# Performance work log

Measured on AMD Instinct MI355X. Metric: run time of the kernel, lower is better.

Reference implementation:

```python
import jax, jax.numpy as jnp
import numpy as np
from jax import lax

M = 5           # top-m similarities per (same/diff) group
MU = 2048       # number of confident target samples kept
K = 10          # top-k src neighbors for pseudo-label voting
NUM_CLASSES = 31
N, D = 4096, 256


def setup_inputs() -> dict:
    key = jax.random.key(0)
    k1, k2, k3 = jax.random.split(key, 3)
    return {
        "src_features": jax.random.normal(k1, (N, D), dtype=jnp.float32),
        "src_labels": jax.random.randint(k2, (N,), 0, NUM_CLASSES),
        "tgt_features": jax.random.normal(k3, (N, D), dtype=jnp.float32),
    }


def _forward(src_features, tgt_features, src_labels):
    # sim = 1 / (cdist(src, tgt) + 1), shape [Ns, Nt]
    sq_s = jnp.sum(src_features * src_features, axis=1, keepdims=True)   # [Ns,1]
    sq_t = jnp.sum(tgt_features * tgt_features, axis=1, keepdims=True)   # [Nt,1]
    d2 = jnp.maximum(sq_s + sq_t.T - 2.0 * (src_features @ tgt_features.T), 0.0)
    sim = 1.0 / (jnp.sqrt(d2) + 1.0)                                     # [Ns,Nt]

    # --- target pseudo-labels: majority vote among top-K most similar src samples per tgt column
    _, top_idx = lax.top_k(sim.T, K)                                     # [Nt,K] over src dim
    top_lab = src_labels[top_idx]                                        # [Nt,K]
    counts = jnp.sum(jax.nn.one_hot(top_lab, NUM_CLASSES, dtype=jnp.float32), axis=1)  # [Nt,C]
    # argmax returns smallest class index on ties, matching torch.mode
    assigned = jnp.argmax(counts, axis=1)                                # [Nt]

    # --- similarity-ratio confidence score per target
    same = src_labels[:, None] == assigned[None, :]                      # [Ns,Nt]
    # sims are strictly positive, so masking with 0 preserves the per-group top-M
    nln_sum = jnp.sum(lax.top_k(jnp.where(same, sim, 0.0).T, M)[0], axis=-1)   # [Nt]
    nun_sum = jnp.sum(lax.top_k(jnp.where(same, 0.0, sim).T, M)[0], axis=-1)   # [Nt]
    score = nln_sum / nun_sum                                            # [Nt]

    # keep MU most confident target columns
    top_tgt = lax.top_k(score, MU)[1]                                    # [MU]
    fsim = sim[:, top_tgt]                                               # [Ns,MU]
    flab = assigned[top_tgt]                                             # [MU]

    # --- masked-softmax contrastive loss
    mask_sim = (src_labels[:, None] == flab[None, :]).astype(jnp.float32)  # [Ns,MU]
    n_same = jnp.sum(mask_sim, axis=1)
    # original keeps rows that have at least one same-label AND one diff-label column;
    # the final_mask broadcasts per-row, so softmax runs over the full row for valid rows
    valid = (n_same > 0.0) & (n_same < float(MU))                        # [Ns]
    p = jax.nn.softmax(fsim, axis=1)
    contr = jnp.sum(p * mask_sim, axis=1)                                # [Ns]
    contr_safe = jnp.where(valid, contr, 1.0)
    n_valid = jnp.sum(valid.astype(jnp.float32))
    loss = -jnp.sum(jnp.where(valid, jnp.log(contr_safe), 0.0)) / n_valid
    return loss


def reference(src_features, src_labels, tgt_features):
    return _forward(src_features, tgt_features, src_labels)
```

## Files before the change

kernel.cpp:

```cpp
#include <hip/hip_runtime.h>
#include <hip/hip_bf16.h>
#include <cfloat>

#define NN 4096
#define DD 256
#define KTOP 10
#define MTOP 5
#define MUSEL 2048
#define NCLS 31

typedef unsigned long long u64;
typedef unsigned int u32;
typedef __attribute__((ext_vector_type(8))) short short8;
typedef __attribute__((ext_vector_type(4))) float f32x4;

static __device__ __forceinline__ unsigned short f2bf(float x) {
    u32 u = __float_as_uint(x);
    u32 r = (u + 0x7FFFu + ((u >> 16) & 1u)) >> 16;
    return (unsigned short)r;
}
static __device__ __forceinline__ float bf2f(unsigned short h) {
    return __uint_as_float((u32)h << 16);
}

template <int C>
static __device__ __forceinline__ u32 dpp_keep(u32 x) {
    return (u32)__builtin_amdgcn_update_dpp((int)x, (int)x, C, 0xF, 0xF, false);
}
template <int C>
static __device__ __forceinline__ u32 dpp_zero(u32 x) {
    return (u32)__builtin_amdgcn_update_dpp(0, (int)x, C, 0xF, 0xF, true);
}
static __device__ __forceinline__ u32 wred_max(u32 x) {
#define S(C) { u32 t = dpp_keep<C>(x); x = t > x ? t : x; }
    S(0x111) S(0x112) S(0x114) S(0x118) S(0x142) S(0x143)
#undef S
    return (u32)__builtin_amdgcn_readlane((int)x, 63);
}
static __device__ __forceinline__ u32 wred_sum_u32(u32 x) {
#define S(C) { u32 t = dpp_zero<C>(x); x += t; }
    S(0x111) S(0x112) S(0x114) S(0x118) S(0x142) S(0x143)
#undef S
    return (u32)__builtin_amdgcn_readlane((int)x, 63);
}
static __device__ __forceinline__ float wred_sumf(float x) {
#define S(C) { u32 t = dpp_zero<C>(__float_as_uint(x)); x += __uint_as_float(t); }
    S(0x111) S(0x112) S(0x114) S(0x118) S(0x142) S(0x143)
#undef S
    return __uint_as_float((u32)__builtin_amdgcn_readlane((int)__float_as_uint(x), 63));
}

static __device__ __forceinline__ void merge_pairs(const u32* pairs, int n, u32 need,
                                                   u32& t, u32& bn, int lane) {
    u32 val = (lane < n) ? pairs[lane * 2] : 0u;
    u32 cnt = (lane < n) ? pairs[lane * 2 + 1] : 0u;
    t = 0u; bn = 0u;
    for (int k = 0; k < 10; ++k) {
        if (need == 0u) break;
        u32 m = wred_max(val);
        if (m == 0u) break;
        u32 c = wred_sum_u32(val == m ? cnt : 0u);
        if (c >= need) { t = m; bn = need; break; }
        need -= c;
        if (val == m) val = 0u;
    }
}

__global__ __launch_bounds__(256) void prep_kernel(const float* __restrict__ src,
                                                   const float* __restrict__ tgt,
                                                   unsigned short* __restrict__ src_hi,
                                                   unsigned short* __restrict__ src_lo,
                                                   unsigned short* __restrict__ tgt_hi,
                                                   unsigned short* __restrict__ tgt_lo,
                                                   float* __restrict__ sq_s,
                                                   float* __restrict__ sq_t) {
    int r = blockIdx.x;
    bool isT = r >= NN;
    int rr = isT ? r - NN : r;
    const float* base = (isT ? tgt : src) + (size_t)rr * DD;
    float x = base[threadIdx.x];
    unsigned short h = f2bf(x);
    unsigned short l = f2bf(x - bf2f(h));
    size_t o = (size_t)rr * DD + threadIdx.x;
    if (isT) { tgt_hi[o] = h; tgt_lo[o] = l; } else { src_hi[o] = h; src_lo[o] = l; }
    float p = x * x;
    for (int off = 32; off > 0; off >>= 1) p += __shfl_down(p, off);
    __shared__ float red[4];
    int wid = threadIdx.x >> 6, lane = threadIdx.x & 63;
    if (lane == 0) red[wid] = p;
    __syncthreads();
    if (threadIdx.x == 0) {
        float s = red[0] + red[1] + red[2] + red[3];
        if (isT) sq_t[rr] = s; else sq_s[rr] = s;
    }
}

static __device__ __forceinline__ void gload(const unsigned short* g, short* l) {
    __builtin_amdgcn_global_load_lds((const __attribute__((address_space(1))) void*)g,
                                     (__attribute__((address_space(3))) void*)l, 16, 0, 0);
}

__global__ __launch_bounds__(256) void gemm_mfma_kernel(
        const unsigned short* __restrict__ tgt_hi, const unsigned short* __restrict__ tgt_lo,
        const unsigned short* __restrict__ src_hi, const unsigned short* __restrict__ src_lo,
        const float* __restrict__ sq_s, const float* __restrict__ sq_t,
        float* __restrict__ simT) {
    __shared__ short Ahi[2][128 * 32];
    __shared__ short Alo[2][128 * 32];
    __shared__ short Bhi[2][128 * 32];
    __shared__ short Blo[2][128 * 32];
    int tid = threadIdx.x;
    int wid = tid >> 6, lane = tid & 63;
    int lin = blockIdx.x;
    int wg = (lin & 7) * 128 + (lin >> 3);
    int i0 = (wg & 31) * 128;
    int j0 = (wg >> 5) * 128;
    int wr = wid >> 1, wc = wid & 1;

    f32x4 acc[4][4];
#pragma unroll
    for (int m = 0; m < 4; ++m)
#pragma unroll
        for (int n = 0; n < 4; ++n) acc[m][n] = (f32x4){0.f, 0.f, 0.f, 0.f};

    int srow = wid * 32 + (lane >> 2);
    int skoff = (lane & 3) * 8;
    int fr = lane & 15;
    int kq = (lane >> 4) * 8;

#define STAGE_SLICE(kk, bb)                                                      \
    {                                                                            \
        _Pragma("unroll")                                                        \
        for (int r = 0; r < 2; ++r) {                                            \
            int row = srow + r * 16;                                             \
            size_t goA = (size_t)(j0 + row) * DD + (kk) + skoff;                 \
            size_t goB = (size_t)(i0 + row) * DD + (kk) + skoff;                 \
            int ldo = (wid * 2 + r) * 512;                                       \
            gload(tgt_hi + goA, Ahi[bb] + ldo);                                  \
            gload(tgt_lo + goA, Alo[bb] + ldo);                                  \
            gload(src_hi + goB, Bhi[bb] + ldo);                                  \
            gload(src_lo + goB, Blo[bb] + ldo);                                  \
        }                                                                        \
    }

    STAGE_SLICE(0, 0);
    __syncthreads();
    int buf = 0;
    for (int t = 0; t < 8; ++t) {
        if (t < 7) STAGE_SLICE((t + 1) * 32, buf ^ 1);
        short8 ah[4], bh[4], bl[4], al[4];
#pragma unroll
        for (int m = 0; m < 4; ++m) {
            int ra = (wr * 64 + m * 16 + fr) * 32 + kq;
            int rb = (wc * 64 + m * 16 + fr) * 32 + kq;
            ah[m] = *(const short8*)(Ahi[buf] + ra);
            bh[m] = *(const short8*)(Bhi[buf] + rb);
        }
#pragma unroll
        for (int m = 0; m < 4; ++m)
#pragma unroll
            for (int n = 0; n < 4; ++n)
                acc[m][n] = __builtin_amdgcn_mfma_f32_16x16x32_bf16(ah[m], bh[n], acc[m][n], 0, 0, 0);
#pragma unroll
        for (int m = 0; m < 4; ++m)
            bl[m] = *(const short8*)(Blo[buf] + (wc * 64 + m * 16 + fr) * 32 + kq);
#pragma unroll
        for (int m = 0; m < 4; ++m)
#pragma unroll
            for (int n = 0; n < 4; ++n)
                acc[m][n] = __builtin_amdgcn_mfma_f32_16x16x32_bf16(ah[m], bl[n], acc[m][n], 0, 0, 0);
#pragma unroll
        for (int m = 0; m < 4; ++m)
            al[m] = *(const short8*)(Alo[buf] + (wr * 64 + m * 16 + fr) * 32 + kq);
#pragma unroll
        for (int m = 0; m < 4; ++m)
#pragma unroll
            for (int n = 0; n < 4; ++n)
                acc[m][n] = __builtin_amdgcn_mfma_f32_16x16x32_bf16(al[m], bh[n], acc[m][n], 0, 0, 0);
        __syncthreads();
        buf ^= 1;
    }
#undef STAGE_SLICE

    int fq = lane >> 4;
#pragma unroll
    for (int m = 0; m < 4; ++m) {
#pragma unroll
        for (int n = 0; n < 4; ++n) {
            int i = i0 + wc * 64 + n * 16 + fr;
            float ss = sq_s[i];
#pragma unroll
            for (int r = 0; r < 4; ++r) {
                int j = j0 + wr * 64 + m * 16 + fq * 4 + r;
                float d2 = fmaxf(ss + sq_t[j] - 2.0f * acc[m][n][r], 0.0f);
                simT[(size_t)j * NN + i] = 1.0f / (sqrtf(d2) + 1.0f);
            }
        }
    }
}

__global__ __launch_bounds__(256) void percol_kernel(const float* __restrict__ simT,
                                                     const int* __restrict__ labels,
                                                     int* __restrict__ assigned,
                                                     float* __restrict__ score) {
    __shared__ u32 pairs1[4][KTOP][2];
    __shared__ u32 pairs2[4][MTOP][2];
    __shared__ u32 pairs3[4][MTOP][2];
    __shared__ u32 votebin[32];
    __shared__ u32 eqlist[64];
    __shared__ u32 s_eqcnt;
    __shared__ u32 s_v10, s_bneed;
    __shared__ u32 s_t2, s_b2, s_t3, s_b3;
    __shared__ float sred2[4], sred3[4];
    int tid = threadIdx.x, lane = tid & 63, wid = tid >> 6;
    int j = blockIdx.x;

    float v[16];
    u32 labp[4];
    {
        const float4* pA = (const float4*)(simT + (size_t)j * NN + tid * 16);
        const int4*  pL = (const int4*)(labels + tid * 16);
#pragma unroll
        for (int q = 0; q < 4; ++q) {
            float4 a = pA[q];
            v[q * 4 + 0] = a.x; v[q * 4 + 1] = a.y; v[q * 4 + 2] = a.z; v[q * 4 + 3] = a.w;
            int4 l = pL[q];
            labp[q] = (u32)l.x | ((u32)l.y << 8) | ((u32)l.z << 16) | ((u32)l.w << 24);
        }
    }
#define LAB(r) ((int)((labp[(r) >> 2] >> (((r) & 3) * 8)) & 0xFFu))
    if (tid < 32) votebin[tid] = 0u;
    if (tid == 0) s_eqcnt = 0u;

    {
        u32 thr = ~0u, need = KTOP;
#pragma unroll
        for (int k = 0; k < KTOP; ++k) {
            u32 lm = 0u;
            if (need) {
#pragma unroll
                for (int r = 0; r < 16; ++r) {
                    u32 b = __float_as_uint(v[r]);
                    if (b < thr && b > lm) lm = b;
                }
            }
            u32 m = wred_max(lm);
            u32 lc = 0u;
            if (m) {
#pragma unroll
                for (int r = 0; r < 16; ++r) lc += (__float_as_uint(v[r]) == m) ? 1u : 0u;
            }
            u32 c = wred_sum_u32(lc);
            if (lane == 0) { pairs1[wid][k][0] = m; pairs1[wid][k][1] = c; }
            need = (m == 0u) ? 0u : ((c >= need) ? 0u : need - c);
            thr = m;
        }
    }
    __syncthreads();
    if (wid == 0) {
        u32 t, bn;
        merge_pairs(&pairs1[0][0][0], 4 * KTOP, KTOP, t, bn, lane);
        if (lane == 0) { s_v10 = t; s_bneed = bn; }
    }
    __syncthreads();
    u32 v10 = s_v10, bneed = s_bneed;

#pragma unroll
    for (int r = 0; r < 16; ++r) {
        u32 b = __float_as_uint(v[r]);
        if (b > v10) atomicAdd(&votebin[LAB(r)], 1u);
        else if (b == v10) {
            u32 p = atomicAdd(&s_eqcnt, 1u);
            if (p < 64u) eqlist[p] = ((u32)(tid * 16 + r) << 8) | (u32)LAB(r);
        }
    }
    __syncthreads();
    if (tid == 0) {
        int ne = (int)min(s_eqcnt, 64u);
        for (u32 k = 0; k < bneed; ++k) {
            u32 best = ~0u; int bi = -1;
            for (int e = 0; e < ne; ++e) if (eqlist[e] < best) { best = eqlist[e]; bi = e; }
            if (bi >= 0) { votebin[best & 0xFFu] += 1u; eqlist[bi] = ~0u; }
        }
    }
    __syncthreads();
    int asg;
    {
        u32 vk = (lane < NCLS) ? ((votebin[lane] << 6) | (u32)(63 - lane)) : 0u;
        vk = wred_max(vk);
        asg = 63 - (int)(vk & 63u);
    }

    u32 sm16 = 0u;
#pragma unroll
    for (int r = 0; r < 16; ++r) if (LAB(r) == asg) sm16 |= 1u << r;
    {
        u32 thr = ~0u, need = MTOP;
#pragma unroll
        for (int k = 0; k < MTOP; ++k) {
            u32 lm = 0u;
            if (need) {
#pragma unroll
                for (int r = 0; r < 16; ++r) {
                    u32 b = __float_as_uint(v[r]);
                    if (((sm16 >> r) & 1u) && b < thr && b > lm) lm = b;
                }
            }
            u32 m = wred_max(lm);
            u32 lc = 0u;
            if (m) {
#pragma unroll
                for (int r = 0; r < 16; ++r)
                    lc += (((sm16 >> r) & 1u) && __float_as_uint(v[r]) == m) ? 1u : 0u;
            }
            u32 c = wred_sum_u32(lc);
            if (lane == 0) { pairs2[wid][k][0] = m; pairs2[wid][k][1] = c; }
            need = (m == 0u) ? 0u : ((c >= need) ? 0u : need - c);
            thr = m;
        }
    }
    {
        u32 thr = ~0u, need = MTOP;
#pragma unroll
        for (int k = 0; k < MTOP; ++k) {
            u32 lm = 0u;
            if (need) {
#pragma unroll
                for (int r = 0; r < 16; ++r) {
                    u32 b = __float_as_uint(v[r]);
                    if (!((sm16 >> r) & 1u) && b < thr && b > lm) lm = b;
                }
            }
            u32 m = wred_max(lm);
            u32 lc = 0u;
            if (m) {
#pragma unroll
                for (int r = 0; r < 16; ++r)
                    lc += (!((sm16 >> r) & 1u) && __float_as_uint(v[r]) == m) ? 1u : 0u;
            }
            u32 c = wred_sum_u32(lc);
            if (lane == 0) { pairs3[wid][k][0] = m; pairs3[wid][k][1] = c; }
            need = (m == 0u) ? 0u : ((c >= need) ? 0u : need - c);
            thr = m;
        }
    }
    __syncthreads();
    if (wid == 0) {
        u32 t, bn;
        merge_pairs(&pairs2[0][0][0], 4 * MTOP, MTOP, t, bn, lane);
        if (lane == 0) { s_t2 = t; s_b2 = bn; }
    }
    if (wid == 1) {
        u32 t, bn;
        merge_pairs(&pairs3[0][0][0], 4 * MTOP, MTOP, t, bn, lane);
        if (lane == 0) { s_t3 = t; s_b3 = bn; }
    }
    __syncthreads();
    u32 t2 = s_t2, b2 = s_b2, t3 = s_t3, b3 = s_b3;

    float s2 = 0.f, s3 = 0.f;
#pragma unroll
    for (int r = 0; r < 16; ++r) {
        u32 b = __float_as_uint(v[r]);
        if ((sm16 >> r) & 1u) { if (b > t2) s2 += v[r]; }
        else                  { if (b > t3) s3 += v[r]; }
    }
    s2 = wred_sumf(s2);
    s3 = wred_sumf(s3);
    if (lane == 0) { sred2[wid] = s2; sred3[wid] = s3; }
    __syncthreads();
    if (tid == 0) {
        float nln = sred2[0] + sred2[1] + sred2[2] + sred2[3] + (float)b2 * __uint_as_float(t2);
        float nun = sred3[0] + sred3[1] + sred3[2] + sred3[3] + (float)b3 * __uint_as_float(t3);
        assigned[j] = asg;
        score[j] = nln / nun;
    }
#undef LAB
}

__global__ __launch_bounds__(1024) void select_kernel(const float* __restrict__ score,
                                                      const int* __restrict__ assigned,
                                                      int* __restrict__ top_tgt,
                                                      int* __restrict__ flab,
                                                      int* __restrict__ histg) {
    __shared__ u64 keys[NN];
    __shared__ __attribute__((aligned(16))) u32 hist[256];
    __shared__ u64 s_prefix;
    __shared__ u32 s_rem;
    __shared__ int hcls[32];
    __shared__ int s_counter;
    int tid = threadIdx.x;
#pragma unroll
    for (int t = 0; t < 4; ++t) {
        int i = t * 1024 + tid;
        keys[i] = ((u64)__float_as_uint(score[i]) << 32) | (u64)(0xFFFFFFFFu - (u32)i);
    }
    if (tid == 0) { s_prefix = 0ull; s_rem = MUSEL; s_counter = 0; }
    if (tid < 32) hcls[tid] = 0;
    if (tid < 256) hist[tid] = 0u;
    __syncthreads();
    for (int pass = 0; pass < 8; ++pass) {
        int shift = 56 - pass * 8;
        u64 pref = s_prefix;
#pragma unroll
        for (int t = 0; t < 4; ++t) {
            u64 k = keys[t * 1024 + tid];
            bool match = (pass == 0) || ((k >> (shift + 8)) == (pref >> (shift + 8)));
            if (match) atomicAdd(&hist[(u32)(k >> shift) & 255u], 1u);
        }
        __syncthreads();
        if (tid < 64) {
            int g = 63 - tid;
            uint4 h = *(uint4*)&hist[4 * g];
            *(uint4*)&hist[4 * g] = make_uint4(0u, 0u, 0u, 0u);
            u32 s = h.x + h.y + h.z + h.w, P = s;
#pragma unroll
            for (int o = 1; o < 64; o <<= 1) { u32 tt = __shfl_up(P, o); if (tid >= o) P += tt; }
            u32 need = s_rem;
            unsigned long long bal = __ballot(P >= need);
            int l0 = __ffsll(bal) - 1;
            u32 c = P - s, b, nn;
            if (c + h.w >= need) { b = 3u; nn = need - c; }
            else { c += h.w; if (c + h.z >= need) { b = 2u; nn = need - c; }
                   else { c += h.z; if (c + h.y >= need) { b = 1u; nn = need - c; }
                          else { c += h.y; b = 0u; nn = need - c; } } }
            if (tid == l0) { s_prefix = pref | ((u64)((u32)(4 * g) + b) << shift); s_rem = nn; }
        }
        __syncthreads();
    }
    u64 thr = s_prefix;
#pragma unroll
    for (int t = 0; t < 4; ++t) {
        int i = t * 1024 + tid;
        if (keys[i] >= thr) {
            int p = atomicAdd(&s_counter, 1);
            int idx = (int)(0xFFFFFFFFu - (u32)(keys[i] & 0xFFFFFFFFull));
            top_tgt[p] = idx;
            int a = assigned[idx];
            flab[p] = a;
            atomicAdd(&hcls[a], 1);
        }
    }
    __syncthreads();
    if (tid < 32) histg[tid] = hcls[tid];
}

#define JCH 64
__global__ __launch_bounds__(256) void fpart_kernel(const float* __restrict__ simT,
                                                    const int* __restrict__ top_tgt,
                                                    const int* __restrict__ flab,
                                                    const int* __restrict__ labels,
                                                    float* __restrict__ ps,
                                                    float* __restrict__ pt) {
    __shared__ int tt[JCH];
    __shared__ int fl[JCH];
    int tid = threadIdx.x;
    int ci = blockIdx.x, cj = blockIdx.y;
    if (tid < JCH) { tt[tid] = top_tgt[cj * JCH + tid]; fl[tid] = flab[cj * JCH + tid]; }
    __syncthreads();
    int i = ci * 256 + tid;
    int myl = labels[i];
    float s = 0.f, t = 0.f;
#pragma unroll 4
    for (int jj = 0; jj < JCH; ++jj) {
        float v = simT[(size_t)tt[jj] * NN + i];
        float e = __expf(v);
        s += e;
        t += (fl[jj] == myl) ? e : 0.f;
    }
    ps[cj * NN + i] = s;
    pt[cj * NN + i] = t;
}

__global__ __launch_bounds__(256) void merge_kernel(const float* __restrict__ ps,
                                                    const float* __restrict__ pt,
                                                    const int* __restrict__ labels,
                                                    const int* __restrict__ hist,
                                                    float* __restrict__ partials) {
    int tid = threadIdx.x;
    int i = blockIdx.x * 256 + tid;
    float S = 0.f, T = 0.f;
#pragma unroll
    for (int c = 0; c < 32; ++c) {
        S += ps[c * NN + i];
        T += pt[c * NN + i];
    }
    float contr = T / S;
    int ns = hist[labels[i]];
    bool valid = (ns > 0) && (ns < MUSEL);
    float term = valid ? __logf(contr) : 0.0f;
    float cnt = valid ? 1.0f : 0.0f;
    for (int off = 32; off > 0; off >>= 1) {
        term += __shfl_down(term, off);
        cnt  += __shfl_down(cnt, off);
    }
    __shared__ float rt[4], rc[4];
    int wid = tid >> 6, lane = tid & 63;
    if (lane == 0) { rt[wid] = term; rc[wid] = cnt; }
    __syncthreads();
    if (tid == 0) {
        partials[blockIdx.x * 2]     = rt[0] + rt[1] + rt[2] + rt[3];
        partials[blockIdx.x * 2 + 1] = rc[0] + rc[1] + rc[2] + rc[3];
    }
}

__global__ void final_kernel(const float* __restrict__ partials, float* __restrict__ out) {
    if (threadIdx.x == 0) {
        float s = 0.f, c = 0.f;
        for (int b = 0; b < 16; ++b) { s += partials[b * 2]; c += partials[b * 2 + 1]; }
        out[0] = -s / c;
    }
}

extern "C" void kernel_launch(void* const* d_in, const int* in_sizes, int n_in,
                              void* d_out, int out_size, void* d_ws, size_t ws_size,
                              hipStream_t stream) {
    const float* src    = (const float*)d_in[0];
    const int*   labels = (const int*)d_in[1];
    const float* tgt    = (const float*)d_in[2];
    float* out = (float*)d_out;

    char* ws = (char*)d_ws;
    size_t off = 0;
    float* simT = (float*)(ws + off);             off += (size_t)NN * NN * sizeof(float);
    unsigned short* tgt_hi = (unsigned short*)(ws + off); off += (size_t)NN * DD * 2;
    unsigned short* tgt_lo = (unsigned short*)(ws + off); off += (size_t)NN * DD * 2;
    unsigned short* src_hi = (unsigned short*)(ws + off); off += (size_t)NN * DD * 2;
    unsigned short* src_lo = (unsigned short*)(ws + off); off += (size_t)NN * DD * 2;
    float* sq_s = (float*)(ws + off);      off += NN * sizeof(float);
    float* sq_t = (float*)(ws + off);      off += NN * sizeof(float);
    float* score = (float*)(ws + off);     off += NN * sizeof(float);
    int*   assigned = (int*)(ws + off);    off += NN * sizeof(int);
    int*   top_tgt = (int*)(ws + off);     off += MUSEL * sizeof(int);
    int*   flab = (int*)(ws + off);        off += MUSEL * sizeof(int);
    int*   hist = (int*)(ws + off);        off += 32 * sizeof(int);
    float* partials = (float*)(ws + off);  off += 32 * sizeof(float);
    float* ps = (float*)tgt_lo;
    float* pt = (float*)src_hi;

    prep_kernel<<<2 * NN, 256, 0, stream>>>(src, tgt, src_hi, src_lo, tgt_hi, tgt_lo, sq_s, sq_t);
    gemm_mfma_kernel<<<1024, 256, 0, stream>>>(tgt_hi, tgt_lo, src_hi, src_lo, sq_s, sq_t, simT);
    percol_kernel<<<NN, 256, 0, stream>>>(simT, labels, assigned, score);
    select_kernel<<<1, 1024, 0, stream>>>(score, assigned, top_tgt, flab, hist);
    fpart_kernel<<<dim3(16, 32), 256, 0, stream>>>(simT, top_tgt, flab, labels, ps, pt);
    merge_kernel<<<16, 256, 0, stream>>>(ps, pt, labels, hist, partials);
    final_kernel<<<1, 64, 0, stream>>>(partials, out);
}
```

Before: 209.1 us.

## Sort per-thread values with bitonic network for top-k; single-buffer GEMM LDS

```diff
diff --git a/kernel.cpp b/kernel.cpp
--- a/kernel.cpp
+++ b/kernel.cpp
@@ -105,10 +105,10 @@
         const unsigned short* __restrict__ src_hi, const unsigned short* __restrict__ src_lo,
         const float* __restrict__ sq_s, const float* __restrict__ sq_t,
         float* __restrict__ simT) {
-    __shared__ short Ahi[2][128 * 32];
-    __shared__ short Alo[2][128 * 32];
-    __shared__ short Bhi[2][128 * 32];
-    __shared__ short Blo[2][128 * 32];
+    __shared__ short Ahi[128 * 32];
+    __shared__ short Alo[128 * 32];
+    __shared__ short Bhi[128 * 32];
+    __shared__ short Blo[128 * 32];
     int tid = threadIdx.x;
     int wid = tid >> 6, lane = tid & 63;
     int lin = blockIdx.x;
@@ -128,33 +128,27 @@
     int fr = lane & 15;
     int kq = (lane >> 4) * 8;
 
-#define STAGE_SLICE(kk, bb)                                                      \
-    {                                                                            \
-        _Pragma("unroll")                                                        \
-        for (int r = 0; r < 2; ++r) {                                            \
-            int row = srow + r * 16;                                             \
-            size_t goA = (size_t)(j0 + row) * DD + (kk) + skoff;                 \
-            size_t goB = (size_t)(i0 + row) * DD + (kk) + skoff;                 \
-            int ldo = (wid * 2 + r) * 512;                                       \
-            gload(tgt_hi + goA, Ahi[bb] + ldo);                                  \
-            gload(tgt_lo + goA, Alo[bb] + ldo);                                  \
-            gload(src_hi + goB, Bhi[bb] + ldo);                                  \
-            gload(src_lo + goB, Blo[bb] + ldo);                                  \
-        }                                                                        \
-    }
-
-    STAGE_SLICE(0, 0);
-    __syncthreads();
-    int buf = 0;
     for (int t = 0; t < 8; ++t) {
-        if (t < 7) STAGE_SLICE((t + 1) * 32, buf ^ 1);
+        int kk = t * 32;
+#pragma unroll
+        for (int r = 0; r < 2; ++r) {
+            int row = srow + r * 16;
+            size_t goA = (size_t)(j0 + row) * DD + kk + skoff;
+            size_t goB = (size_t)(i0 + row) * DD + kk + skoff;
+            int ldo = (wid * 2 + r) * 512;
+            gload(tgt_hi + goA, Ahi + ldo);
+            gload(tgt_lo + goA, Alo + ldo);
+            gload(src_hi + goB, Bhi + ldo);
+            gload(src_lo + goB, Blo + ldo);
+        }
+        __syncthreads();
         short8 ah[4], bh[4], bl[4], al[4];
 #pragma unroll
         for (int m = 0; m < 4; ++m) {
             int ra = (wr * 64 + m * 16 + fr) * 32 + kq;
             int rb = (wc * 64 + m * 16 + fr) * 32 + kq;
-            ah[m] = *(const short8*)(Ahi[buf] + ra);
-            bh[m] = *(const short8*)(Bhi[buf] + rb);
+            ah[m] = *(const short8*)(Ahi + ra);
+            bh[m] = *(const short8*)(Bhi + rb);
         }
 #pragma unroll
         for (int m = 0; m < 4; ++m)
@@ -163,7 +157,7 @@
                 acc[m][n] = __builtin_amdgcn_mfma_f32_16x16x32_bf16(ah[m], bh[n], acc[m][n], 0, 0, 0);
 #pragma unroll
         for (int m = 0; m < 4; ++m)
-            bl[m] = *(const short8*)(Blo[buf] + (wc * 64 + m * 16 + fr) * 32 + kq);
+            bl[m] = *(const short8*)(Blo + (wc * 64 + m * 16 + fr) * 32 + kq);
 #pragma unroll
         for (int m = 0; m < 4; ++m)
 #pragma unroll
@@ -171,16 +165,14 @@
                 acc[m][n] = __builtin_amdgcn_mfma_f32_16x16x32_bf16(ah[m], bl[n], acc[m][n], 0, 0, 0);
 #pragma unroll
         for (int m = 0; m < 4; ++m)
-            al[m] = *(const short8*)(Alo[buf] + (wr * 64 + m * 16 + fr) * 32 + kq);
+            al[m] = *(const short8*)(Alo + (wr * 64 + m * 16 + fr) * 32 + kq);
 #pragma unroll
         for (int m = 0; m < 4; ++m)
 #pragma unroll
             for (int n = 0; n < 4; ++n)
                 acc[m][n] = __builtin_amdgcn_mfma_f32_16x16x32_bf16(al[m], bh[n], acc[m][n], 0, 0, 0);
         __syncthreads();
-        buf ^= 1;
-    }
-#undef STAGE_SLICE
+    }
 
     int fq = lane >> 4;
 #pragma unroll
@@ -198,6 +190,37 @@
         }
     }
 }
+
+#define CED(X,Y) { u32 mx_ = X > Y ? X : Y; u32 mn_ = X > Y ? Y : X; X = mx_; Y = mn_; }
+#define CEA(X,Y) { u32 mx_ = X > Y ? X : Y; u32 mn_ = X > Y ? Y : X; X = mn_; Y = mx_; }
+#define SORT16_DESC()                                                                         \
+    CED(a0,a1) CEA(a2,a3) CED(a4,a5) CEA(a6,a7) CED(a8,a9) CEA(a10,a11) CED(a12,a13) CEA(a14,a15) \
+    CED(a0,a2) CED(a1,a3) CEA(a4,a6) CEA(a5,a7) CED(a8,a10) CED(a9,a11) CEA(a12,a14) CEA(a13,a15) \
+    CED(a0,a1) CED(a2,a3) CEA(a4,a5) CEA(a6,a7) CED(a8,a9) CED(a10,a11) CEA(a12,a13) CEA(a14,a15) \
+    CED(a0,a4) CED(a1,a5) CED(a2,a6) CED(a3,a7) CEA(a8,a12) CEA(a9,a13) CEA(a10,a14) CEA(a11,a15) \
+    CED(a0,a2) CED(a1,a3) CED(a4,a6) CED(a5,a7) CEA(a8,a10) CEA(a9,a11) CEA(a12,a14) CEA(a13,a15) \
+    CED(a0,a1) CED(a2,a3) CED(a4,a5) CED(a6,a7) CEA(a8,a9) CEA(a10,a11) CEA(a12,a13) CEA(a14,a15) \
+    CED(a0,a8) CED(a1,a9) CED(a2,a10) CED(a3,a11) CED(a4,a12) CED(a5,a13) CED(a6,a14) CED(a7,a15) \
+    CED(a0,a4) CED(a1,a5) CED(a2,a6) CED(a3,a7) CED(a8,a12) CED(a9,a13) CED(a10,a14) CED(a11,a15) \
+    CED(a0,a2) CED(a1,a3) CED(a4,a6) CED(a5,a7) CED(a8,a10) CED(a9,a11) CED(a12,a14) CED(a13,a15) \
+    CED(a0,a1) CED(a2,a3) CED(a4,a5) CED(a6,a7) CED(a8,a9) CED(a10,a11) CED(a12,a13) CED(a14,a15)
+#define SHIFT15() { a0=a1;a1=a2;a2=a3;a3=a4;a4=a5;a5=a6;a6=a7;a7=a8;a8=a9;a9=a10;a10=a11;a11=a12;a12=a13;a13=a14;a14=a15;a15=0u; }
+#define SETA(F) { a0=F(0);a1=F(1);a2=F(2);a3=F(3);a4=F(4);a5=F(5);a6=F(6);a7=F(7); \
+                  a8=F(8);a9=F(9);a10=F(10);a11=F(11);a12=F(12);a13=F(13);a14=F(14);a15=F(15); }
+#define EXTRACT(PAIRS, NEEDK, ROUNDS)                                     \
+    {                                                                     \
+        u32 need_ = NEEDK;                                                \
+        for (int k_ = 0; k_ < ROUNDS; ++k_) {                             \
+            u32 m_ = wred_max(a0);                                        \
+            if (m_ == 0u) break;                                          \
+            unsigned long long bal_ = __ballot(a0 == m_);                 \
+            u32 c_ = (u32)__popcll(bal_);                                 \
+            if (lane == 0) { PAIRS[k_][0] = m_; PAIRS[k_][1] = c_; }      \
+            if (a0 == m_) SHIFT15()                                       \
+            if (c_ >= need_) break;                                       \
+            need_ -= c_;                                                  \
+        }                                                                 \
+    }
 
 __global__ __launch_bounds__(256) void percol_kernel(const float* __restrict__ simT,
                                                      const int* __restrict__ labels,
@@ -231,31 +254,18 @@
 #define LAB(r) ((int)((labp[(r) >> 2] >> (((r) & 3) * 8)) & 0xFFu))
     if (tid < 32) votebin[tid] = 0u;
     if (tid == 0) s_eqcnt = 0u;
-
-    {
-        u32 thr = ~0u, need = KTOP;
-#pragma unroll
-        for (int k = 0; k < KTOP; ++k) {
-            u32 lm = 0u;
-            if (need) {
-#pragma unroll
-                for (int r = 0; r < 16; ++r) {
-                    u32 b = __float_as_uint(v[r]);
-                    if (b < thr && b > lm) lm = b;
-                }
-            }
-            u32 m = wred_max(lm);
-            u32 lc = 0u;
-            if (m) {
-#pragma unroll
-                for (int r = 0; r < 16; ++r) lc += (__float_as_uint(v[r]) == m) ? 1u : 0u;
-            }
-            u32 c = wred_sum_u32(lc);
-            if (lane == 0) { pairs1[wid][k][0] = m; pairs1[wid][k][1] = c; }
-            need = (m == 0u) ? 0u : ((c >= need) ? 0u : need - c);
-            thr = m;
-        }
-    }
+    if (lane < KTOP) { pairs1[wid][lane][0] = 0u; pairs1[wid][lane][1] = 0u; }
+    if (lane < MTOP) {
+        pairs2[wid][lane][0] = 0u; pairs2[wid][lane][1] = 0u;
+        pairs3[wid][lane][0] = 0u; pairs3[wid][lane][1] = 0u;
+    }
+
+    u32 a0, a1, a2, a3, a4, a5, a6, a7, a8, a9, a10, a11, a12, a13, a14, a15;
+
+#define BITS(r) __float_as_uint(v[r])
+    SETA(BITS)
+    SORT16_DESC()
+    EXTRACT(pairs1[wid], KTOP, KTOP)
     __syncthreads();
     if (wid == 0) {
         u32 t, bn;
@@ -294,56 +304,17 @@
     u32 sm16 = 0u;
 #pragma unroll
     for (int r = 0; r < 16; ++r) if (LAB(r) == asg) sm16 |= 1u << r;
-    {
-        u32 thr = ~0u, need = MTOP;
-#pragma unroll
-        for (int k = 0; k < MTOP; ++k) {
-            u32 lm = 0u;
-            if (need) {
-#pragma unroll
-                for (int r = 0; r < 16; ++r) {
-                    u32 b = __float_as_uint(v[r]);
-                    if (((sm16 >> r) & 1u) && b < thr && b > lm) lm = b;
-                }
-            }
-            u32 m = wred_max(lm);
-            u32 lc = 0u;
-            if (m) {
-#pragma unroll
-                for (int r = 0; r < 16; ++r)
-                    lc += (((sm16 >> r) & 1u) && __float_as_uint(v[r]) == m) ? 1u : 0u;
-            }
-            u32 c = wred_sum_u32(lc);
-            if (lane == 0) { pairs2[wid][k][0] = m; pairs2[wid][k][1] = c; }
-            need = (m == 0u) ? 0u : ((c >= need) ? 0u : need - c);
-            thr = m;
-        }
-    }
-    {
-        u32 thr = ~0u, need = MTOP;
-#pragma unroll
-        for (int k = 0; k < MTOP; ++k) {
-            u32 lm = 0u;
-            if (need) {
-#pragma unroll
-                for (int r = 0; r < 16; ++r) {
-                    u32 b = __float_as_uint(v[r]);
-                    if (!((sm16 >> r) & 1u) && b < thr && b > lm) lm = b;
-                }
-            }
-            u32 m = wred_max(lm);
-            u32 lc = 0u;
-            if (m) {
-#pragma unroll
-                for (int r = 0; r < 16; ++r)
-                    lc += (!((sm16 >> r) & 1u) && __float_as_uint(v[r]) == m) ? 1u : 0u;
-            }
-            u32 c = wred_sum_u32(lc);
-            if (lane == 0) { pairs3[wid][k][0] = m; pairs3[wid][k][1] = c; }
-            need = (m == 0u) ? 0u : ((c >= need) ? 0u : need - c);
-            thr = m;
-        }
-    }
+
+#define BITS2(r) ((((sm16 >> (r)) & 1u)) ? __float_as_uint(v[r]) : 0u)
+    SETA(BITS2)
+    SORT16_DESC()
+    EXTRACT(pairs2[wid], MTOP, MTOP)
+
+#define BITS3(r) ((((sm16 >> (r)) & 1u)) ? 0u : __float_as_uint(v[r]))
+    SETA(BITS3)
+    SORT16_DESC()
+    EXTRACT(pairs3[wid], MTOP, MTOP)
+
     __syncthreads();
     if (wid == 0) {
         u32 t, bn;
@@ -376,6 +347,9 @@
         score[j] = nln / nun;
     }
 #undef LAB
+#undef BITS
+#undef BITS2
+#undef BITS3
 }
 
 __global__ __launch_bounds__(1024) void select_kernel(const float* __restrict__ score,
```

Result: faster. 172.6 us (-17.5%).
